# Optimization experiments

Hardware: AMD Instinct MI355X
Metric: run time of the kernel (lower is better)

Reference implementation:

```python
import jax, jax.numpy as jnp
import numpy as np

B, L, C = 1, 1536, 768
H, DK, DV, F = 8, 64, 96, 96


def setup_inputs() -> dict:
    key = jax.random.key(0)
    ks = jax.random.split(key, 9)
    s = 0.02
    return {
        "x": jax.random.normal(ks[0], (B, L, C), jnp.float32),
        "Wq": jax.random.normal(ks[1], (C, H * DK), jnp.float32) * s,
        "Wk": jax.random.normal(ks[2], (C, H * DK), jnp.float32) * s,
        "Wv": jax.random.normal(ks[3], (C, H * DV), jnp.float32) * s,
        "Wout": jax.random.normal(ks[4], (H * DV, C), jnp.float32) * s,
        "bout": jnp.zeros((C,), jnp.float32),
        "Wpos": jax.random.normal(ks[5], (F, H * DK), jnp.float32) * s,
        "rel_content_bias": jax.random.normal(ks[6], (1, H, 1, DK), jnp.float32),
        "rel_pos_bias": jax.random.normal(ks[7], (1, H, 1, DK), jnp.float32),
    }


def central_mask_embed(n, features):
    # positions: -(n-1) .. n-1  -> (2n-1,)
    positions = jnp.arange(-(n - 1), n)
    # center widths: 2^1 - 1 .. 2^features - 1
    widths = jnp.float32(2.0) ** jnp.arange(1, features + 1, dtype=jnp.float32) - 1.0
    return (widths[None, :] > jnp.abs(positions).astype(jnp.float32)[:, None]).astype(jnp.float32)


def relative_shift(t):
    # t: (b, h, t1, t2) with t2 = 2*t1 - 1 -> (b, h, t1, t1)
    b, h, t1, t2 = t.shape
    t = jnp.pad(t, ((0, 0), (0, 0), (0, 0), (1, 0)))  # (b,h,t1,t2+1)
    t = t.reshape(b, h, t2 + 1, t1)[:, :, 1:, :]       # (b,h,t2,t1)
    t = t.reshape(b, h, t1, t2)
    return t[..., : (t2 + 2) // 2]


def reference(x, Wq, Wk, Wv, Wout, bout, Wpos, rel_content_bias, rel_pos_bias):
    b, n, _ = x.shape
    q = (x @ Wq).reshape(b, n, H, DK).transpose(0, 2, 1, 3)  # b h n d
    k = (x @ Wk).reshape(b, n, H, DK).transpose(0, 2, 1, 3)
    v = (x @ Wv).reshape(b, n, H, DV).transpose(0, 2, 1, 3)
    q = q / jnp.float32(DK) ** 0.5

    content_logits = jnp.einsum("bhid,bhjd->bhij", q + rel_content_bias, k)

    pos = central_mask_embed(n, F)                 # (2n-1, F)
    pos_k = (pos @ Wpos).reshape(2 * n - 1, H, DK).transpose(1, 0, 2)  # h (2n-1) d
    pos_logits = jnp.einsum("bhid,hjd->bhij", q + rel_pos_bias, pos_k)
    pos_logits = relative_shift(pos_logits)        # (b,h,n,n)

    attn = jax.nn.softmax(content_logits + pos_logits, axis=-1)
    out = jnp.einsum("bhij,bhjd->bhid", attn, v)   # b h n dv
    out = out.transpose(0, 2, 1, 3).reshape(b, n, H * DV)
    return out @ Wout + bout
```

## Files before the change

kernel.cpp:

```cpp
#include <hip/hip_runtime.h>
#include <stdint.h>

#define NTOK 1536
#define CDIM 768
#define NH 8
#define DKH 64
#define DVH 96
#define NF 96

typedef unsigned short u16;
typedef __attribute__((ext_vector_type(8))) short s16x8;
typedef __attribute__((ext_vector_type(4))) float f32x4;

__device__ __forceinline__ float b2f(u16 u) {
    union { uint32_t i; float f; } v; v.i = ((uint32_t)u) << 16; return v.f;
}
__device__ __forceinline__ u16 f2b(float f) {
    union { float f; uint32_t i; } v; v.f = f;
    uint32_t x = v.i;
    return (u16)((x + 0x7FFFu + ((x >> 16) & 1u)) >> 16);
}
__device__ __forceinline__ float ldin(const void* p, int i, int f32) {
    return f32 ? ((const float*)p)[i] : b2f(((const u16*)p)[i]);
}

__device__ __forceinline__ int probe_f32(const void* p) {
    const u16* a = (const u16*)p;
    int lane = threadIdx.x & 63;
    int bad = 0;
#pragma unroll
    for (int t = 0; t < 4; ++t) {
        float v = b2f(a[lane + t * 64]);
        if (!(fabsf(v) < 1e6f)) bad = 1;
    }
    return __ballot(bad) != 0ull;
}

#define FIDX(m, kk) ((((kk) >> 3) * 16 + (m)) * 8 + ((kk) & 7))

#define OFF_WSUF 16
#define OFF_S11  (OFF_WSUF + 5632)
#define OFF_QF   (OFF_S11 + 147456)
#define OFF_KF   (OFF_QF + 393216)
#define OFF_VF   (OFF_KF + 393216)
#define OFF_AOF  (OFF_VF + 589824)
#define OFF_XF   (OFF_AOF + 589824)
#define OFF_WF   (OFF_XF + 589824)
#define OFF_WOF  (OFF_WF + 688128)

__global__ __launch_bounds__(256) void prep(const void* __restrict__ x,
                                            const void* __restrict__ Wq,
                                            const void* __restrict__ Wk,
                                            const void* __restrict__ Wv,
                                            const void* __restrict__ Wout,
                                            const void* __restrict__ Wpos,
                                            float* __restrict__ ws) {
    int bx = blockIdx.x, tid = threadIdx.x;
    int wv = tid >> 6, L = tid & 63;

    if (bx < 144) {
        int f = probe_f32(x);
        u16* dst = (u16*)(ws + OFF_XF);
        int cbase = (bx * 4 + wv) * 4;
        int m = L & 15, kq = L >> 4;
        int srcs[4];
#pragma unroll
        for (int c = 0; c < 4; ++c) {
            int ch = cbase + c;
            int ti = ch / 24, kc = ch % 24;
            srcs[c] = (ti * 16 + m) * CDIM + kc * 32 + kq * 8;
        }
        if (f) {
            float4 a[4][2];
#pragma unroll
            for (int c = 0; c < 4; ++c) {
                const float* xp = (const float*)x + srcs[c];
                a[c][0] = *(const float4*)(xp);
                a[c][1] = *(const float4*)(xp + 4);
            }
#pragma unroll
            for (int c = 0; c < 4; ++c) {
                union { u16 u[8]; uint4 v; } pk;
                pk.u[0] = f2b(a[c][0].x); pk.u[1] = f2b(a[c][0].y);
                pk.u[2] = f2b(a[c][0].z); pk.u[3] = f2b(a[c][0].w);
                pk.u[4] = f2b(a[c][1].x); pk.u[5] = f2b(a[c][1].y);
                pk.u[6] = f2b(a[c][1].z); pk.u[7] = f2b(a[c][1].w);
                *(uint4*)(dst + (cbase + c) * 512 + L * 8) = pk.v;
            }
        } else {
            uint4 v[4];
#pragma unroll
            for (int c = 0; c < 4; ++c) v[c] = *(const uint4*)((const u16*)x + srcs[c]);
#pragma unroll
            for (int c = 0; c < 4; ++c)
                *(uint4*)(dst + (cbase + c) * 512 + L * 8) = v[c];
        }
        return;
    }
    if (bx < 1104) {
        int c = (bx - 144) * 4 + wv;
        const void* src; int ld, cn0; u16* dst; int kc;
        if (c < 2688) {
            int tn = c / 24; kc = c % 24;
            int n0 = tn * 16;
            dst = (u16*)(ws + OFF_WF) + c * 512;
            if (n0 < 512)       { src = Wq; ld = 512;  cn0 = n0; }
            else if (n0 < 1024) { src = Wk; ld = 512;  cn0 = n0 - 512; }
            else                { src = Wv; ld = CDIM; cn0 = n0 - 1024; }
        } else {
            int c2 = c - 2688;
            int tn = c2 / 24; kc = c2 % 24;
            dst = (u16*)(ws + OFF_WOF) + c2 * 512;
            src = Wout; ld = CDIM; cn0 = tn * 16;
        }
        int f = probe_f32(src);
        int nn = L & 15, kq = L >> 4;
        int base = (kc * 32 + kq * 8) * ld + cn0 + nn;
        union { u16 u[8]; uint4 v; } pk;
        if (f) {
            const float* sp = (const float*)src + base;
            float a0 = sp[0], a1 = sp[ld], a2 = sp[2 * ld], a3 = sp[3 * ld];
            float a4 = sp[4 * ld], a5 = sp[5 * ld], a6 = sp[6 * ld], a7 = sp[7 * ld];
            pk.u[0] = f2b(a0); pk.u[1] = f2b(a1); pk.u[2] = f2b(a2); pk.u[3] = f2b(a3);
            pk.u[4] = f2b(a4); pk.u[5] = f2b(a5); pk.u[6] = f2b(a6); pk.u[7] = f2b(a7);
        } else {
            const u16* sp = (const u16*)src + base;
            pk.u[0] = sp[0]; pk.u[1] = sp[ld]; pk.u[2] = sp[2 * ld]; pk.u[3] = sp[3 * ld];
            pk.u[4] = sp[4 * ld]; pk.u[5] = sp[5 * ld]; pk.u[6] = sp[6 * ld]; pk.u[7] = sp[7 * ld];
        }
        *(uint4*)(dst + L * 8) = pk.v;
        return;
    }
    int t = bx - 1104;
    int f = probe_f32(Wpos);
    for (int hd = tid; hd < 512; hd += 256) {
        float s0 = 0.f, s1 = 0.f, s2 = 0.f, s3 = 0.f;
        int f0 = t;
        for (; f0 + 4 <= NF; f0 += 4) {
            s0 += ldin(Wpos, f0 * 512 + hd, f);
            s1 += ldin(Wpos, (f0 + 1) * 512 + hd, f);
            s2 += ldin(Wpos, (f0 + 2) * 512 + hd, f);
            s3 += ldin(Wpos, (f0 + 3) * 512 + hd, f);
        }
        for (; f0 < NF; ++f0) s0 += ldin(Wpos, f0 * 512 + hd, f);
        ws[OFF_WSUF + t * 512 + hd] = (s0 + s1) + (s2 + s3);
    }
}

__global__ __launch_bounds__(256) void qkv_reg(const void* __restrict__ rcb,
                                               const void* __restrict__ rpb,
                                               float* __restrict__ ws) {
    __shared__ float qt[64 * 68];
    __shared__ float rpd[12];
    const u16* xf = (const u16*)(ws + OFF_XF);
    const u16* wf = (const u16*)(ws + OFF_WF);
    u16* qf = (u16*)(ws + OFF_QF);
    u16* kf = (u16*)(ws + OFF_KF);
    u16* vf = (u16*)(ws + OFF_VF);

    int tid = threadIdx.x;
    int lane = tid & 63, w = tid >> 6;
    int quad = lane >> 4, col = lane & 15;
    int ti4 = blockIdx.x;
    int tn4 = blockIdx.y;
    int tn = tn4 * 4 + w;
    int i0 = ti4 * 64;
    bool isQ = (tn4 < 8);
    int hq = tn4;

    s16x8 bw0, bw1;
    int f32p = 0, f32c = 0;
    if (isQ) {
        f32p = probe_f32(rpb);
        f32c = probe_f32(rcb);
        int t = lane & 15, kq = lane >> 4;
        union { u16 u[8]; s16x8 v; } p0, p1;
#pragma unroll
        for (int j = 0; j < 8; ++j) {
            float v0 = 0.f, v1 = 0.f;
            if (t < 11) {
                v0 = ws[OFF_WSUF + t * 512 + hq * 64 + kq * 8 + j];
                v1 = ws[OFF_WSUF + t * 512 + hq * 64 + 32 + kq * 8 + j];
            }
            p0.u[j] = f2b(v0); p1.u[j] = f2b(v1);
        }
        bw0 = p0.v; bw1 = p1.v;
        if (tid < 12) {
            float s = 0.f;
            if (tid < 11) {
                const float* wp = ws + OFF_WSUF + tid * 512 + hq * 64;
                for (int d = 0; d < 64; ++d) s += ldin(rpb, hq * 64 + d, f32p) * wp[d];
            }
            rpd[tid] = s;
        }
    }

    f32x4 acc[4];
#pragma unroll
    for (int mt = 0; mt < 4; ++mt) acc[mt] = (f32x4){0.f, 0.f, 0.f, 0.f};

    const u16* bp = wf + (tn * 24) * 512 + lane * 8;
    const u16* ap = xf + (ti4 * 4 * 24) * 512 + lane * 8;
#pragma unroll 4
    for (int kc = 0; kc < 24; ++kc) {
        s16x8 bfrag = *(const s16x8*)(bp + kc * 512);
#pragma unroll
        for (int mt = 0; mt < 4; ++mt) {
            s16x8 afrag = *(const s16x8*)(ap + (mt * 24 + kc) * 512);
            acc[mt] = __builtin_amdgcn_mfma_f32_16x16x32_bf16(afrag, bfrag, acc[mt], 0, 0, 0);
        }
    }

    if (isQ) {
#pragma unroll
        for (int mt = 0; mt < 4; ++mt)
#pragma unroll
            for (int r = 0; r < 4; ++r)
                qt[(mt * 16 + quad * 4 + r) * 68 + w * 16 + col] = acc[mt][r] * 0.125f;
        __syncthreads();
        int m = lane & 15, kq = lane >> 4;
#pragma unroll
        for (int kc2 = 0; kc2 < 2; ++kc2) {
            union { u16 u[8]; uint4 v; } pk;
#pragma unroll
            for (int j = 0; j < 8; ++j) {
                int d = kc2 * 32 + kq * 8 + j;
                pk.u[j] = f2b(qt[(w * 16 + m) * 68 + d] + ldin(rcb, hq * 64 + d, f32c));
            }
            *(uint4*)(qf + (((hq * 96 + ti4 * 4 + w) * 2 + kc2) * 512) + lane * 8) = pk.v;
        }
        union { u16 u[8]; s16x8 v; } qa0, qa1;
#pragma unroll
        for (int j = 0; j < 8; ++j) {
            qa0.u[j] = f2b(qt[(w * 16 + m) * 68 + kq * 8 + j]);
            qa1.u[j] = f2b(qt[(w * 16 + m) * 68 + 32 + kq * 8 + j]);
        }
        f32x4 s11a = (f32x4){0.f, 0.f, 0.f, 0.f};
        s11a = __builtin_amdgcn_mfma_f32_16x16x32_bf16(qa0.v, bw0, s11a, 0, 0, 0);
        s11a = __builtin_amdgcn_mfma_f32_16x16x32_bf16(qa1.v, bw1, s11a, 0, 0, 0);
        if (col < 12) {
            float rp = rpd[col];
            float* s11 = ws + OFF_S11;
#pragma unroll
            for (int r = 0; r < 4; ++r)
                s11[(hq * NTOK + i0 + w * 16 + quad * 4 + r) * 12 + col] = s11a[r] + rp;
        }
    } else if (tn < 64) {
        int h = (tn >> 2) - 8;
        int d = ((tn & 3) * 16) + col;
#pragma unroll
        for (int mt = 0; mt < 4; ++mt) {
            int tj = ti4 * 4 + mt;
#pragma unroll
            for (int r = 0; r < 4; ++r) {
                int nn = quad * 4 + r;
                kf[((h * 96 + tj) * 2 + (d >> 5)) * 512 + FIDX(nn, d & 31)] = f2b(acc[mt][r]);
            }
        }
    } else {
        int c = tn * 16 + col - 1024;
        int h = c / 96, d = c % 96;
        int nt = d >> 4, nn = d & 15;
#pragma unroll
        for (int mt = 0; mt < 4; ++mt) {
#pragma unroll
            for (int r = 0; r < 4; ++r) {
                int j = i0 + mt * 16 + quad * 4 + r;
                int jc = j >> 5, kk = j & 31;
// ... 96 lines not shown
        pa.u2[1] = *(const uint2*)(pr + 4);
        const u16* vp = vf + ((h * 48 + jc) * 6) * 512 + lane * 8;
#pragma unroll
        for (int nt = 0; nt < 6; ++nt) {
            s16x8 vfr = *(const s16x8*)(vp + nt * 512);
            O[nt] = __builtin_amdgcn_mfma_f32_16x16x32_bf16(pa.v, vfr, O[nt], 0, 0, 0);
        }
    }

#pragma unroll
    for (int off = 1; off < 16; off <<= 1)
#pragma unroll
        for (int r = 0; r < 4; ++r) lsum[r] += __shfl_xor(lsum[r], off);
    if (col == 0)
#pragma unroll
        for (int r = 0; r < 4; ++r) lw[wv][quad * 4 + r] = lsum[r];
#pragma unroll
    for (int r = 0; r < 4; ++r) {
        int row = quad * 4 + r;
#pragma unroll
        for (int nt = 0; nt < 6; ++nt)
            Om[wv][row * 96 + nt * 16 + col] = O[nt][r];
    }
    __syncthreads();
    for (int idx = tid; idx < 16 * 96; idx += 512) {
        int row = idx / 96, cc = idx % 96;
        float L = 0.f, val = 0.f;
#pragma unroll
        for (int v = 0; v < 8; ++v) { L += lw[v][row]; val += Om[v][idx]; }
        aof[(ti * 24 + h * 3 + (cc >> 5)) * 512 + FIDX(row, cc & 31)] = f2b(val / L);
    }
}

__global__ __launch_bounds__(256) void out_reg(const void* __restrict__ bout,
                                               float* __restrict__ ws,
                                               float* __restrict__ out) {
    const u16* af = (const u16*)(ws + OFF_AOF);
    const u16* wof = (const u16*)(ws + OFF_WOF);
    int f32b = probe_f32(bout);

    int tid = threadIdx.x;
    int lane = tid & 63, w = tid >> 6;
    int quad = lane >> 4, col = lane & 15;
    int ti4 = blockIdx.x;
    int tn = blockIdx.y * 4 + w;
    int i0 = ti4 * 64;
    int n0 = blockIdx.y * 64;

    f32x4 acc[4];
#pragma unroll
    for (int mt = 0; mt < 4; ++mt) acc[mt] = (f32x4){0.f, 0.f, 0.f, 0.f};

    const u16* bp = wof + (tn * 24) * 512 + lane * 8;
    const u16* ap = af + (ti4 * 4 * 24) * 512 + lane * 8;
#pragma unroll 4
    for (int kc = 0; kc < 24; ++kc) {
        s16x8 bfrag = *(const s16x8*)(bp + kc * 512);
#pragma unroll
        for (int mt = 0; mt < 4; ++mt) {
            s16x8 afrag = *(const s16x8*)(ap + (mt * 24 + kc) * 512);
            acc[mt] = __builtin_amdgcn_mfma_f32_16x16x32_bf16(afrag, bfrag, acc[mt], 0, 0, 0);
        }
    }

    int c = n0 + w * 16 + col;
    float bias = ldin(bout, c, f32b);
#pragma unroll
    for (int mt = 0; mt < 4; ++mt) {
#pragma unroll
        for (int r = 0; r < 4; ++r) {
            int i = i0 + mt * 16 + quad * 4 + r;
            out[i * CDIM + c] = acc[mt][r] + bias;
        }
    }
}

extern "C" void kernel_launch(void* const* d_in, const int* in_sizes, int n_in,
                              void* d_out, int out_size, void* d_ws, size_t ws_size,
                              hipStream_t stream) {
    float* out = (float*)d_out;
    float* ws = (float*)d_ws;

    const int want[9] = {1179648, 393216, 393216, 589824, 589824, 768, 49152, 512, 512};
    int role2in[9], used[9] = {0};
    bool ok = (n_in == 9);
    if (ok) {
        for (int r = 0; r < 9; ++r) {
            int found = -1;
            for (int i = 0; i < 9 && found < 0; ++i)
                if (!used[i] && in_sizes[i] == want[r]) found = i;
            if (found < 0) { ok = false; break; }
            used[found] = 1;
            role2in[r] = found;
        }
    }
    if (!ok) for (int r = 0; r < 9; ++r) role2in[r] = r;

    const void* x    = d_in[role2in[0]];
    const void* Wq   = d_in[role2in[1]];
    const void* Wk   = d_in[role2in[2]];
    const void* Wv   = d_in[role2in[3]];
    const void* Wout = d_in[role2in[4]];
    const void* bout = d_in[role2in[5]];
    const void* Wpos = d_in[role2in[6]];
    const void* rcb  = d_in[role2in[7]];
    const void* rpb  = d_in[role2in[8]];

    hipLaunchKernelGGL(prep, dim3(1115), dim3(256), 0, stream,
                       x, Wq, Wk, Wv, Wout, Wpos, ws);
    hipLaunchKernelGGL(qkv_reg, dim3(24, 28), dim3(256), 0, stream,
                       rcb, rpb, ws);
    hipLaunchKernelGGL(attn_mfma, dim3(768), dim3(512), 0, stream, ws);
    hipLaunchKernelGGL(out_reg, dim3(24, 12), dim3(256), 0, stream,
                       bout, ws, out);
}
```

Before: 147.2 us.

## Fuse four kernels into two cooperative kernels with grid-wide syncs

Replaces the prep+qkv and attention+out-projection kernel pairs with two persistent cooperative kernels that loop over work units and use a grid sync between phases, falling back to the original launches if cooperative launch fails. The aim is to cut kernel launch gaps and tail effects between dependent stages. In exchange, grids are capped at occupancy times CU count, so work is serialized through grid-stride loops, and grid.sync adds its own barrier cost. Device properties and occupancy are queried once and cached in statics.

```diff
diff --git a/kernel.cpp b/kernel.cpp
--- a/kernel.cpp
+++ b/kernel.cpp
@@ -1,5 +1,8 @@
 #include <hip/hip_runtime.h>
+#include <hip/hip_cooperative_groups.h>
 #include <stdint.h>
+
+namespace cg = cooperative_groups;
 
 #define NTOK 1536
 #define CDIM 768
@@ -439,6 +442,406 @@
     }
 }
 
+__global__ __launch_bounds__(256) void fused_pq(const void* __restrict__ x,
+                                                const void* __restrict__ Wq,
+                                                const void* __restrict__ Wk,
+                                                const void* __restrict__ Wv,
+                                                const void* __restrict__ Wout,
+                                                const void* __restrict__ Wpos,
+                                                const void* __restrict__ rcb,
+                                                const void* __restrict__ rpb,
+                                                float* __restrict__ ws) {
+    __shared__ float qt[64 * 68];
+    __shared__ float rpd[12];
+    int tid = threadIdx.x;
+    int wv = tid >> 6, L = tid & 63;
+
+    for (int u = blockIdx.x; u < 1115; u += gridDim.x) {
+        if (u < 144) {
+            int f = probe_f32(x);
+            u16* dst = (u16*)(ws + OFF_XF);
+            int cbase = (u * 4 + wv) * 4;
+            int m = L & 15, kq = L >> 4;
+            int srcs[4];
+#pragma unroll
+            for (int c = 0; c < 4; ++c) {
+                int ch = cbase + c;
+                int ti = ch / 24, kc = ch % 24;
+                srcs[c] = (ti * 16 + m) * CDIM + kc * 32 + kq * 8;
+            }
+            if (f) {
+                float4 a[4][2];
+#pragma unroll
+                for (int c = 0; c < 4; ++c) {
+                    const float* xp = (const float*)x + srcs[c];
+                    a[c][0] = *(const float4*)(xp);
+                    a[c][1] = *(const float4*)(xp + 4);
+                }
+#pragma unroll
+                for (int c = 0; c < 4; ++c) {
+                    union { u16 uu[8]; uint4 v; } pk;
+                    pk.uu[0] = f2b(a[c][0].x); pk.uu[1] = f2b(a[c][0].y);
+                    pk.uu[2] = f2b(a[c][0].z); pk.uu[3] = f2b(a[c][0].w);
+                    pk.uu[4] = f2b(a[c][1].x); pk.uu[5] = f2b(a[c][1].y);
+                    pk.uu[6] = f2b(a[c][1].z); pk.uu[7] = f2b(a[c][1].w);
+                    *(uint4*)(dst + (cbase + c) * 512 + L * 8) = pk.v;
+                }
+            } else {
+                uint4 v[4];
+#pragma unroll
+                for (int c = 0; c < 4; ++c) v[c] = *(const uint4*)((const u16*)x + srcs[c]);
+#pragma unroll
+                for (int c = 0; c < 4; ++c)
+                    *(uint4*)(dst + (cbase + c) * 512 + L * 8) = v[c];
+            }
+        } else if (u < 1104) {
+            int c = (u - 144) * 4 + wv;
+            const void* src; int ld, cn0; u16* dst; int kc;
+            if (c < 2688) {
+                int tn = c / 24; kc = c % 24;
+                int n0 = tn * 16;
+                dst = (u16*)(ws + OFF_WF) + c * 512;
+                if (n0 < 512)       { src = Wq; ld = 512;  cn0 = n0; }
+                else if (n0 < 1024) { src = Wk; ld = 512;  cn0 = n0 - 512; }
+                else                { src = Wv; ld = CDIM; cn0 = n0 - 1024; }
+            } else {
+                int c2 = c - 2688;
+                int tn = c2 / 24; kc = c2 % 24;
+                dst = (u16*)(ws + OFF_WOF) + c2 * 512;
+                src = Wout; ld = CDIM; cn0 = tn * 16;
+            }
+            int f = probe_f32(src);
+            int nn = L & 15, kq = L >> 4;
+            int base = (kc * 32 + kq * 8) * ld + cn0 + nn;
+            union { u16 uu[8]; uint4 v; } pk;
+            if (f) {
+                const float* sp = (const float*)src + base;
+                float a0 = sp[0], a1 = sp[ld], a2 = sp[2 * ld], a3 = sp[3 * ld];
+                float a4 = sp[4 * ld], a5 = sp[5 * ld], a6 = sp[6 * ld], a7 = sp[7 * ld];
+                pk.uu[0] = f2b(a0); pk.uu[1] = f2b(a1); pk.uu[2] = f2b(a2); pk.uu[3] = f2b(a3);
+                pk.uu[4] = f2b(a4); pk.uu[5] = f2b(a5); pk.uu[6] = f2b(a6); pk.uu[7] = f2b(a7);
+            } else {
+                const u16* sp = (const u16*)src + base;
+                pk.uu[0] = sp[0]; pk.uu[1] = sp[ld]; pk.uu[2] = sp[2 * ld]; pk.uu[3] = sp[3 * ld];
+                pk.uu[4] = sp[4 * ld]; pk.uu[5] = sp[5 * ld]; pk.uu[6] = sp[6 * ld]; pk.uu[7] = sp[7 * ld];
+            }
+            *(uint4*)(dst + L * 8) = pk.v;
+        } else {
+            int t = u - 1104;
+            int f = probe_f32(Wpos);
+            for (int hd = tid; hd < 512; hd += 256) {
+                float s0 = 0.f, s1 = 0.f, s2 = 0.f, s3 = 0.f;
+                int f0 = t;
+                for (; f0 + 4 <= NF; f0 += 4) {
+                    s0 += ldin(Wpos, f0 * 512 + hd, f);
+                    s1 += ldin(Wpos, (f0 + 1) * 512 + hd, f);
+                    s2 += ldin(Wpos, (f0 + 2) * 512 + hd, f);
+                    s3 += ldin(Wpos, (f0 + 3) * 512 + hd, f);
+                }
+                for (; f0 < NF; ++f0) s0 += ldin(Wpos, f0 * 512 + hd, f);
+                ws[OFF_WSUF + t * 512 + hd] = (s0 + s1) + (s2 + s3);
+            }
+        }
+    }
+
+    __threadfence();
+    cg::this_grid().sync();
+
+    const u16* xf = (const u16*)(ws + OFF_XF);
+    const u16* wf = (const u16*)(ws + OFF_WF);
+    u16* qf = (u16*)(ws + OFF_QF);
+    u16* kf = (u16*)(ws + OFF_KF);
+    u16* vf = (u16*)(ws + OFF_VF);
+
+    for (int u = blockIdx.x; u < 672; u += gridDim.x) {
+        int ti4 = u % 24, tn4 = u / 24;
+        int lane = L, w = wv;
+        int quad = lane >> 4, col = lane & 15;
+        int tn = tn4 * 4 + w;
+        int i0 = ti4 * 64;
+        bool isQ = (tn4 < 8);
+        int hq = tn4;
+
+        s16x8 bw0, bw1;
+        int f32p = 0, f32c = 0;
+        if (isQ) {
+            f32p = probe_f32(rpb);
+            f32c = probe_f32(rcb);
+            int t = lane & 15, kq = lane >> 4;
+            union { u16 uu[8]; s16x8 v; } p0, p1;
+#pragma unroll
+            for (int j = 0; j < 8; ++j) {
+                float v0 = 0.f, v1 = 0.f;
+                if (t < 11) {
+                    v0 = ws[OFF_WSUF + t * 512 + hq * 64 + kq * 8 + j];
+                    v1 = ws[OFF_WSUF + t * 512 + hq * 64 + 32 + kq * 8 + j];
+                }
+                p0.uu[j] = f2b(v0); p1.uu[j] = f2b(v1);
+            }
+            bw0 = p0.v; bw1 = p1.v;
+            if (tid < 12) {
+                float s = 0.f;
+                if (tid < 11) {
+                    const float* wp = ws + OFF_WSUF + tid * 512 + hq * 64;
+                    for (int d = 0; d < 64; ++d) s += ldin(rpb, hq * 64 + d, f32p) * wp[d];
+                }
+                rpd[tid] = s;
+            }
+        }
+
+        f32x4 acc[4];
+#pragma unroll
+        for (int mt = 0; mt < 4; ++mt) acc[mt] = (f32x4){0.f, 0.f, 0.f, 0.f};
+
+        const u16* bp = wf + (tn * 24) * 512 + lane * 8;
+        const u16* ap = xf + (ti4 * 4 * 24) * 512 + lane * 8;
+#pragma unroll 4
+        for (int kc = 0; kc < 24; ++kc) {
+            s16x8 bfrag = *(const s16x8*)(bp + kc * 512);
+#pragma unroll
+            for (int mt = 0; mt < 4; ++mt) {
+                s16x8 afrag = *(const s16x8*)(ap + (mt * 24 + kc) * 512);
+                acc[mt] = __builtin_amdgcn_mfma_f32_16x16x32_bf16(afrag, bfrag, acc[mt], 0, 0, 0);
+            }
+        }
+
+        if (isQ) {
+#pragma unroll
+            for (int mt = 0; mt < 4; ++mt)
+#pragma unroll
+                for (int r = 0; r < 4; ++r)
+                    qt[(mt * 16 + quad * 4 + r) * 68 + w * 16 + col] = acc[mt][r] * 0.125f;
+            __syncthreads();
+            int m = lane & 15, kq = lane >> 4;
+#pragma unroll
+            for (int kc2 = 0; kc2 < 2; ++kc2) {
+                union { u16 uu[8]; uint4 v; } pk;
+#pragma unroll
+                for (int j = 0; j < 8; ++j) {
+                    int d = kc2 * 32 + kq * 8 + j;
+                    pk.uu[j] = f2b(qt[(w * 16 + m) * 68 + d] + ldin(rcb, hq * 64 + d, f32c));
+                }
+                *(uint4*)(qf + (((hq * 96 + ti4 * 4 + w) * 2 + kc2) * 512) + lane * 8) = pk.v;
+            }
+            union { u16 uu[8]; s16x8 v; } qa0, qa1;
+#pragma unroll
+            for (int j = 0; j < 8; ++j) {
+                qa0.uu[j] = f2b(qt[(w * 16 + m) * 68 + kq * 8 + j]);
+                qa1.uu[j] = f2b(qt[(w * 16 + m) * 68 + 32 + kq * 8 + j]);
+            }
+            f32x4 s11a = (f32x4){0.f, 0.f, 0.f, 0.f};
+            s11a = __builtin_amdgcn_mfma_f32_16x16x32_bf16(qa0.v, bw0, s11a, 0, 0, 0);
+            s11a = __builtin_amdgcn_mfma_f32_16x16x32_bf16(qa1.v, bw1, s11a, 0, 0, 0);
+            if (col < 12) {
+                float rp = rpd[col];
+                float* s11 = ws + OFF_S11;
+#pragma unroll
+                for (int r = 0; r < 4; ++r)
+                    s11[(hq * NTOK + i0 + w * 16 + quad * 4 + r) * 12 + col] = s11a[r] + rp;
+            }
+        } else if (tn < 64) {
+            int h = (tn >> 2) - 8;
+            int d = ((tn & 3) * 16) + col;
+#pragma unroll
+            for (int mt = 0; mt < 4; ++mt) {
+                int tj = ti4 * 4 + mt;
+#pragma unroll
+                for (int r = 0; r < 4; ++r) {
+                    int nn = quad * 4 + r;
+                    kf[((h * 96 + tj) * 2 + (d >> 5)) * 512 + FIDX(nn, d & 31)] = f2b(acc[mt][r]);
+                }
+            }
+        } else {
+            int c = tn * 16 + col - 1024;
+            int h = c / 96, d = c % 96;
+            int nt = d >> 4, nn = d & 15;
+#pragma unroll
+            for (int mt = 0; mt < 4; ++mt) {
+#pragma unroll
+                for (int r = 0; r < 4; ++r) {
+                    int j = i0 + mt * 16 + quad * 4 + r;
+                    int jc = j >> 5, kk = j & 31;
+                    vf[((h * 48 + jc) * 6 + nt) * 512 + FIDX(nn, kk)] = f2b(acc[mt][r]);
+                }
+            }
+        }
+        if (isQ) __syncthreads();
+    }
+}
+
+__global__ __launch_bounds__(512) void fused_ao(const void* __restrict__ bout,
+                                                float* __restrict__ ws,
+                                                float* __restrict__ out) {
+    __shared__ float s11b[192];
+    __shared__ alignas(16) u16 pbuf[8][16 * 36];
+    __shared__ float Om[8][16 * 96];
+    __shared__ float lw[8][16];
+
+    const u16* qf = (const u16*)(ws + OFF_QF);
+    const u16* kf = (const u16*)(ws + OFF_KF);
+    const u16* vf = (const u16*)(ws + OFF_VF);
+    const float* s11 = ws + OFF_S11;
+    u16* aof = (u16*)(ws + OFF_AOF);
+
+    int tid = threadIdx.x;
+    int wv = tid >> 6, lane = tid & 63;
+    int quad = lane >> 4, col = lane & 15;
+
+    for (int u = blockIdx.x; u < 768; u += gridDim.x) {
+        int h = u & 7;
+        int ti = u >> 3;
+        int i0 = ti * 16;
+
+        if (tid < 192) s11b[tid] = s11[(h * NTOK + i0 + tid / 12) * 12 + tid % 12];
+        const u16* qp = qf + ((h * 96 + ti) * 2) * 512 + lane * 8;
+        s16x8 a_lo = *(const s16x8*)(qp);
+        s16x8 a_hi = *(const s16x8*)(qp + 512);
+        __syncthreads();
+
+        f32x4 O[6];
+        float lsum[4];
+#pragma unroll
+        for (int nt = 0; nt < 6; ++nt) O[nt] = (f32x4){0.f, 0.f, 0.f, 0.f};
+#pragma unroll
+        for (int r = 0; r < 4; ++r) lsum[r] = 0.f;
+
+        const u16* kbase = kf + ((h * 96 + wv * 12) * 2) * 512 + lane * 8;
+        s16x8 k0lo = *(const s16x8*)(kbase);
+        s16x8 k0hi = *(const s16x8*)(kbase + 512);
+        s16x8 k1lo = *(const s16x8*)(kbase + 1024);
+        s16x8 k1hi = *(const s16x8*)(kbase + 1536);
+
+        for (int c = 0; c < 6; ++c) {
+            f32x4 t0 = (f32x4){0.f, 0.f, 0.f, 0.f};
+            f32x4 t1 = (f32x4){0.f, 0.f, 0.f, 0.f};
+            t0 = __builtin_amdgcn_mfma_f32_16x16x32_bf16(a_lo, k0lo, t0, 0, 0, 0);
+            t0 = __builtin_amdgcn_mfma_f32_16x16x32_bf16(a_hi, k0hi, t0, 0, 0, 0);
+            t1 = __builtin_amdgcn_mfma_f32_16x16x32_bf16(a_lo, k1lo, t1, 0, 0, 0);
+            t1 = __builtin_amdgcn_mfma_f32_16x16x32_bf16(a_hi, k1hi, t1, 0, 0, 0);
+            if (c < 5) {
+                const u16* kn = kbase + (c + 1) * 2048;
+                k0lo = *(const s16x8*)(kn);
+                k0hi = *(const s16x8*)(kn + 512);
+                k1lo = *(const s16x8*)(kn + 1024);
+                k1hi = *(const s16x8*)(kn + 1536);
+            }
+            int j0 = wv * 192 + c * 32;
+            int lo1 = j0 - (i0 + 15), lo2 = i0 - (j0 + 31);
+            int dmin = lo1 > 0 ? lo1 : (lo2 > 0 ? lo2 : 0);
+            int dm1 = i0 + 15 - j0, dm2 = j0 + 31 - i0;
+            int dmax = dm1 > dm2 ? dm1 : dm2;
+            int tlo = 31 - __builtin_clz(dmin + 1);
+            int thi = 31 - __builtin_clz(dmax + 1);
+            if (tlo == thi) {
+#pragma unroll
+                for (int r = 0; r < 4; ++r) {
+                    int row = quad * 4 + r;
+                    float bv = s11b[row * 12 + tlo] - 12.f;
+                    float p0 = __expf(t0[r] + bv);
+                    float p1 = __expf(t1[r] + bv);
+                    pbuf[wv][row * 36 + col] = f2b(p0);
+                    pbuf[wv][row * 36 + 16 + col] = f2b(p1);
+                    lsum[r] += p0 + p1;
+                }
+            } else {
+#pragma unroll
+                for (int r = 0; r < 4; ++r) {
+                    int row = quad * 4 + r;
+                    int ig = i0 + row;
+                    int d0 = ig - (j0 + col); d0 = d0 < 0 ? -d0 : d0;
+                    int d1 = ig - (j0 + 16 + col); d1 = d1 < 0 ? -d1 : d1;
+                    float v0 = t0[r] + s11b[row * 12 + (31 - __builtin_clz(d0 + 1))];
+                    float v1 = t1[r] + s11b[row * 12 + (31 - __builtin_clz(d1 + 1))];
+                    float p0 = __expf(v0 - 12.f);
+                    float p1 = __expf(v1 - 12.f);
+                    pbuf[wv][row * 36 + col] = f2b(p0);
+                    pbuf[wv][row * 36 + 16 + col] = f2b(p1);
+                    lsum[r] += p0 + p1;
+                }
+            }
+            int jc = wv * 6 + c;
+            const u16* pr = &pbuf[wv][col * 36 + quad * 8];
+            union { s16x8 v; uint2 u2[2]; } pa;
+            pa.u2[0] = *(const uint2*)(pr);
+            pa.u2[1] = *(const uint2*)(pr + 4);
+            const u16* vp = vf + ((h * 48 + jc) * 6) * 512 + lane * 8;
+#pragma unroll
+            for (int nt = 0; nt < 6; ++nt) {
+                s16x8 vfr = *(const s16x8*)(vp + nt * 512);
+                O[nt] = __builtin_amdgcn_mfma_f32_16x16x32_bf16(pa.v, vfr, O[nt], 0, 0, 0);
+            }
+        }
+
+#pragma unroll
+        for (int off = 1; off < 16; off <<= 1)
+#pragma unroll
+            for (int r = 0; r < 4; ++r) lsum[r] += __shfl_xor(lsum[r], off);
+        if (col == 0)
+#pragma unroll
+            for (int r = 0; r < 4; ++r) lw[wv][quad * 4 + r] = lsum[r];
+#pragma unroll
+        for (int r = 0; r < 4; ++r) {
+            int row = quad * 4 + r;
+#pragma unroll
+            for (int nt = 0; nt < 6; ++nt)
+                Om[wv][row * 96 + nt * 16 + col] = O[nt][r];
+        }
+        __syncthreads();
+        for (int idx = tid; idx < 16 * 96; idx += 512) {
+            int row = idx / 96, cc = idx % 96;
+            float Ls = 0.f, val = 0.f;
+#pragma unroll
+            for (int v = 0; v < 8; ++v) { Ls += lw[v][row]; val += Om[v][idx]; }
+            aof[(ti * 24 + h * 3 + (cc >> 5)) * 512 + FIDX(row, cc & 31)] = f2b(val / Ls);
+        }
+        __syncthreads();
+    }
+
+    __threadfence();
+    cg::this_grid().sync();
+
+    const u16* af = (const u16*)(ws + OFF_AOF);
+    const u16* wof = (const u16*)(ws + OFF_WOF);
+    int f32b = probe_f32(bout);
+    int half = tid >> 8, t2 = tid & 255;
+
+    for (int u = blockIdx.x * 2 + half; u < 288; u += gridDim.x * 2) {
+        int ti4 = u % 24, by = u / 24;
+        int lane2 = t2 & 63, w2 = t2 >> 6;
+        int quad2 = lane2 >> 4, col2 = lane2 & 15;
+        int tn = by * 4 + w2;
+        int i0 = ti4 * 64;
+        int n0 = by * 64;
+
+        f32x4 acc[4];
+#pragma unroll
+        for (int mt = 0; mt < 4; ++mt) acc[mt] = (f32x4){0.f, 0.f, 0.f, 0.f};
+
+        const u16* bp = wof + (tn * 24) * 512 + lane2 * 8;
+        const u16* ap = af + (ti4 * 4 * 24) * 512 + lane2 * 8;
+#pragma unroll 4
+        for (int kc = 0; kc < 24; ++kc) {
+            s16x8 bfrag = *(const s16x8*)(bp + kc * 512);
+#pragma unroll
+            for (int mt = 0; mt < 4; ++mt) {
+                s16x8 afrag = *(const s16x8*)(ap + (mt * 24 + kc) * 512);
+                acc[mt] = __builtin_amdgcn_mfma_f32_16x16x32_bf16(afrag, bfrag, acc[mt], 0, 0, 0);
+            }
+        }
+
+        int c = n0 + w2 * 16 + col2;
+        float bias = ldin(bout, c, f32b);
+#pragma unroll
+        for (int mt = 0; mt < 4; ++mt) {
+#pragma unroll
+            for (int r = 0; r < 4; ++r) {
+                int i = i0 + mt * 16 + quad2 * 4 + r;
+                out[i * CDIM + c] = acc[mt][r] + bias;
+            }
+        }
+    }
+}
+
 extern "C" void kernel_launch(void* const* d_in, const int* in_sizes, int n_in,
                               void* d_out, int out_size, void* d_ws, size_t ws_size,
                               hipStream_t stream) {
@@ -470,11 +873,44 @@
     const void* rcb  = d_in[role2in[7]];
     const void* rpb  = d_in[role2in[8]];
 
-    hipLaunchKernelGGL(prep, dim3(1115), dim3(256), 0, stream,
-                       x, Wq, Wk, Wv, Wout, Wpos, ws);
-    hipLaunchKernelGGL(qkv_reg, dim3(24, 28), dim3(256), 0, stream,
-                       rcb, rpb, ws);
-    hipLaunchKernelGGL(attn_mfma, dim3(768), dim3(512), 0, stream, ws);
-    hipLaunchKernelGGL(out_reg, dim3(24, 12), dim3(256), 0, stream,
-                       bout, ws, out);
-}
+    static int inited = 0;
+    static int nCU = 256, occA = 0, occB = 0;
+    if (!inited) {
+        hipDeviceProp_t prop;
+        int dev = 0;
+        (void)hipGetDevice(&dev);
+        if (hipGetDeviceProperties(&prop, dev) == hipSuccess && prop.multiProcessorCount > 0)
+            nCU = prop.multiProcessorCount;
+        if (hipOccupancyMaxActiveBlocksPerMultiprocessor(&occA, fused_pq, 256, 0) != hipSuccess)
+            occA = 0;
+        if (hipOccupancyMaxActiveBlocksPerMultiprocessor(&occB, fused_ao, 512, 0) != hipSuccess)
+            occB = 0;
+        inited = 1;
+    }
+
+    bool doneA = false, doneB = false;
+    if (occA > 0) {
+        int gridA = occA * nCU; if (gridA > 1115) gridA = 1115;
+        void* argsA[] = {(void*)&x, (void*)&Wq, (void*)&Wk, (void*)&Wv, (void*)&Wout,
+                         (void*)&Wpos, (void*)&rcb, (void*)&rpb, (void*)&ws};
+        doneA = hipLaunchCooperativeKernel(fused_pq, dim3(gridA), dim3(256),
+                                           argsA, 0, stream) == hipSuccess;
+    }
+    if (!doneA) {
+        hipLaunchKernelGGL(prep, dim3(1115), dim3(256), 0, stream,
+                           x, Wq, Wk, Wv, Wout, Wpos, ws);
+        hipLaunchKernelGGL(qkv_reg, dim3(24, 28), dim3(256), 0, stream,
+                           rcb, rpb, ws);
+    }
+    if (occB > 0) {
+        int gridB = occB * nCU; if (gridB > 768) gridB = 768;
+        void* argsB[] = {(void*)&bout, (void*)&ws, (void*)&out};
+        doneB = hipLaunchCooperativeKernel(fused_ao, dim3(gridB), dim3(512),
+                                           argsB, 0, stream) == hipSuccess;
+    }
+    if (!doneB) {
+        hipLaunchKernelGGL(attn_mfma, dim3(768), dim3(512), 0, stream, ws);
+        hipLaunchKernelGGL(out_reg, dim3(24, 12), dim3(256), 0, stream,
+                           bout, ws, out);
+    }
+}
```

Result: slower. 389.0 us (+164.3%).

## Fuse input conversion and positional suffix sums into projection kernels, drop prep

Applied to the files above, without the earlier changes.

Removes the separate prep kernel that converted x and the weights into fragment-ordered bf16 buffers and computed the Wpos suffix sums. The QKV and output projection kernels now load fp32 inputs directly, converting them to bf16 MFMA fragments on the fly with strided loads. The Q blocks recompute the Wpos suffix sums in shared memory. This saves one launch and a workspace round trip, but repeats the conversion per block and uses uncoalesced strided weight loads in the inner loop.

```diff
diff --git a/kernel.cpp b/kernel.cpp
--- a/kernel.cpp
+++ b/kernel.cpp
@@ -38,122 +38,62 @@
 
 #define FIDX(m, kk) ((((kk) >> 3) * 16 + (m)) * 8 + ((kk) & 7))
 
-#define OFF_WSUF 16
-#define OFF_S11  (OFF_WSUF + 5632)
+#define OFF_S11  16
 #define OFF_QF   (OFF_S11 + 147456)
 #define OFF_KF   (OFF_QF + 393216)
 #define OFF_VF   (OFF_KF + 393216)
 #define OFF_AOF  (OFF_VF + 589824)
-#define OFF_XF   (OFF_AOF + 589824)
-#define OFF_WF   (OFF_XF + 589824)
-#define OFF_WOF  (OFF_WF + 688128)
-
-__global__ __launch_bounds__(256) void prep(const void* __restrict__ x,
-                                            const void* __restrict__ Wq,
-                                            const void* __restrict__ Wk,
-                                            const void* __restrict__ Wv,
-                                            const void* __restrict__ Wout,
-                                            const void* __restrict__ Wpos,
-                                            float* __restrict__ ws) {
-    int bx = blockIdx.x, tid = threadIdx.x;
-    int wv = tid >> 6, L = tid & 63;
-
-    if (bx < 144) {
-        int f = probe_f32(x);
-        u16* dst = (u16*)(ws + OFF_XF);
-        int cbase = (bx * 4 + wv) * 4;
-        int m = L & 15, kq = L >> 4;
-        int srcs[4];
-#pragma unroll
-        for (int c = 0; c < 4; ++c) {
-            int ch = cbase + c;
-            int ti = ch / 24, kc = ch % 24;
-            srcs[c] = (ti * 16 + m) * CDIM + kc * 32 + kq * 8;
-        }
-        if (f) {
-            float4 a[4][2];
-#pragma unroll
-            for (int c = 0; c < 4; ++c) {
-                const float* xp = (const float*)x + srcs[c];
-                a[c][0] = *(const float4*)(xp);
-                a[c][1] = *(const float4*)(xp + 4);
-            }
-#pragma unroll
-            for (int c = 0; c < 4; ++c) {
-                union { u16 u[8]; uint4 v; } pk;
-                pk.u[0] = f2b(a[c][0].x); pk.u[1] = f2b(a[c][0].y);
-                pk.u[2] = f2b(a[c][0].z); pk.u[3] = f2b(a[c][0].w);
-                pk.u[4] = f2b(a[c][1].x); pk.u[5] = f2b(a[c][1].y);
-                pk.u[6] = f2b(a[c][1].z); pk.u[7] = f2b(a[c][1].w);
-                *(uint4*)(dst + (cbase + c) * 512 + L * 8) = pk.v;
-            }
-        } else {
-            uint4 v[4];
-#pragma unroll
-            for (int c = 0; c < 4; ++c) v[c] = *(const uint4*)((const u16*)x + srcs[c]);
-#pragma unroll
-            for (int c = 0; c < 4; ++c)
-                *(uint4*)(dst + (cbase + c) * 512 + L * 8) = v[c];
-        }
-        return;
-    }
-    if (bx < 1104) {
-        int c = (bx - 144) * 4 + wv;
-        const void* src; int ld, cn0; u16* dst; int kc;
-        if (c < 2688) {
-            int tn = c / 24; kc = c % 24;
-            int n0 = tn * 16;
-            dst = (u16*)(ws + OFF_WF) + c * 512;
-            if (n0 < 512)       { src = Wq; ld = 512;  cn0 = n0; }
-            else if (n0 < 1024) { src = Wk; ld = 512;  cn0 = n0 - 512; }
-            else                { src = Wv; ld = CDIM; cn0 = n0 - 1024; }
-        } else {
-            int c2 = c - 2688;
-            int tn = c2 / 24; kc = c2 % 24;
-            dst = (u16*)(ws + OFF_WOF) + c2 * 512;
-            src = Wout; ld = CDIM; cn0 = tn * 16;
-        }
-        int f = probe_f32(src);
-        int nn = L & 15, kq = L >> 4;
-        int base = (kc * 32 + kq * 8) * ld + cn0 + nn;
-        union { u16 u[8]; uint4 v; } pk;
-        if (f) {
-            const float* sp = (const float*)src + base;
-            float a0 = sp[0], a1 = sp[ld], a2 = sp[2 * ld], a3 = sp[3 * ld];
-            float a4 = sp[4 * ld], a5 = sp[5 * ld], a6 = sp[6 * ld], a7 = sp[7 * ld];
-            pk.u[0] = f2b(a0); pk.u[1] = f2b(a1); pk.u[2] = f2b(a2); pk.u[3] = f2b(a3);
-            pk.u[4] = f2b(a4); pk.u[5] = f2b(a5); pk.u[6] = f2b(a6); pk.u[7] = f2b(a7);
-        } else {
-            const u16* sp = (const u16*)src + base;
-            pk.u[0] = sp[0]; pk.u[1] = sp[ld]; pk.u[2] = sp[2 * ld]; pk.u[3] = sp[3 * ld];
-            pk.u[4] = sp[4 * ld]; pk.u[5] = sp[5 * ld]; pk.u[6] = sp[6 * ld]; pk.u[7] = sp[7 * ld];
-        }
-        *(uint4*)(dst + L * 8) = pk.v;
-        return;
-    }
-    int t = bx - 1104;
-    int f = probe_f32(Wpos);
-    for (int hd = tid; hd < 512; hd += 256) {
-        float s0 = 0.f, s1 = 0.f, s2 = 0.f, s3 = 0.f;
-        int f0 = t;
-        for (; f0 + 4 <= NF; f0 += 4) {
-            s0 += ldin(Wpos, f0 * 512 + hd, f);
-            s1 += ldin(Wpos, (f0 + 1) * 512 + hd, f);
-            s2 += ldin(Wpos, (f0 + 2) * 512 + hd, f);
-            s3 += ldin(Wpos, (f0 + 3) * 512 + hd, f);
-        }
-        for (; f0 < NF; ++f0) s0 += ldin(Wpos, f0 * 512 + hd, f);
-        ws[OFF_WSUF + t * 512 + hd] = (s0 + s1) + (s2 + s3);
-    }
-}
-
-__global__ __launch_bounds__(256) void qkv_reg(const void* __restrict__ rcb,
-                                               const void* __restrict__ rpb,
-                                               float* __restrict__ ws) {
+
+__device__ __forceinline__ s16x8 ldfragA(const void* x, int f32, int row16,
+                                         int kc, int lane) {
+    int m = lane & 15, kq = lane >> 4;
+    int src = (row16 * 16 + m) * CDIM + kc * 32 + kq * 8;
+    union { u16 uu[8]; uint4 v; s16x8 s; } pk;
+    if (f32) {
+        const float* xp = (const float*)x + src;
+        float4 a0 = *(const float4*)(xp);
+        float4 a1 = *(const float4*)(xp + 4);
+        pk.uu[0] = f2b(a0.x); pk.uu[1] = f2b(a0.y);
+        pk.uu[2] = f2b(a0.z); pk.uu[3] = f2b(a0.w);
+        pk.uu[4] = f2b(a1.x); pk.uu[5] = f2b(a1.y);
+        pk.uu[6] = f2b(a1.z); pk.uu[7] = f2b(a1.w);
+    } else {
+        pk.v = *(const uint4*)((const u16*)x + src);
+    }
+    return pk.s;
+}
+
+__device__ __forceinline__ s16x8 ldfragB(const void* src, int f32, int ld,
+                                         int cn0, int kc, int lane) {
+    int nn = lane & 15, kq = lane >> 4;
+    int base = (kc * 32 + kq * 8) * ld + cn0 + nn;
+    union { u16 uu[8]; s16x8 s; } pk;
+    if (f32) {
+        const float* sp = (const float*)src + base;
+#pragma unroll
+        for (int j = 0; j < 8; ++j) pk.uu[j] = f2b(sp[j * ld]);
+    } else {
+        const u16* sp = (const u16*)src + base;
+#pragma unroll
+        for (int j = 0; j < 8; ++j) pk.uu[j] = sp[j * ld];
+    }
+    return pk.s;
+}
+
+__global__ __launch_bounds__(256) void qkv_self(const void* __restrict__ x,
+                                                const void* __restrict__ Wq,
+                                                const void* __restrict__ Wk,
+                                                const void* __restrict__ Wv,
+                                                const void* __restrict__ Wpos,
+                                                const void* __restrict__ rcb,
+                                                const void* __restrict__ rpb,
+                                                float* __restrict__ ws) {
     __shared__ float qt[64 * 68];
     __shared__ float rpd[12];
-    const u16* xf = (const u16*)(ws + OFF_XF);
-    const u16* wf = (const u16*)(ws + OFF_WF);
+    __shared__ float suf0[11][64];
+    __shared__ float partw[3][64];
+    __shared__ float wsufl[11][64];
+
     u16* qf = (u16*)(ws + OFF_QF);
     u16* kf = (u16*)(ws + OFF_KF);
     u16* vf = (u16*)(ws + OFF_VF);
@@ -168,28 +108,59 @@
     bool isQ = (tn4 < 8);
     int hq = tn4;
 
+    int fx = probe_f32(x);
+
+    const void* bsrc; int bld, bcn0;
+    if (tn < 32)      { bsrc = Wq; bld = 512;  bcn0 = tn * 16; }
+    else if (tn < 64) { bsrc = Wk; bld = 512;  bcn0 = (tn - 32) * 16; }
+    else              { bsrc = Wv; bld = CDIM; bcn0 = (tn - 64) * 16; }
+    int fB = probe_f32(bsrc);
+
     s16x8 bw0, bw1;
     int f32p = 0, f32c = 0;
     if (isQ) {
+        int fwp = probe_f32(Wpos);
         f32p = probe_f32(rpb);
         f32c = probe_f32(rcb);
+        int d = lane;
+        int base = hq * 64 + d;
+        if (w == 0) {
+            float s = 0.f;
+            for (int f0 = 23; f0 >= 0; --f0) {
+                s += ldin(Wpos, f0 * 512 + base, fwp);
+                if (f0 < 11) suf0[f0][d] = s;
+            }
+        } else {
+            float s = 0.f;
+#pragma unroll 4
+            for (int f0 = w * 24; f0 < w * 24 + 24; ++f0)
+                s += ldin(Wpos, f0 * 512 + base, fwp);
+            partw[w - 1][d] = s;
+        }
+        __syncthreads();
+        for (int idx = tid; idx < 11 * 64; idx += 256) {
+            int t = idx >> 6, dd = idx & 63;
+            wsufl[t][dd] = suf0[t][dd] + partw[0][dd] + partw[1][dd] + partw[2][dd];
+        }
+        __syncthreads();
+
         int t = lane & 15, kq = lane >> 4;
-        union { u16 u[8]; s16x8 v; } p0, p1;
+        union { u16 uu[8]; s16x8 v; } p0, p1;
 #pragma unroll
         for (int j = 0; j < 8; ++j) {
             float v0 = 0.f, v1 = 0.f;
             if (t < 11) {
-                v0 = ws[OFF_WSUF + t * 512 + hq * 64 + kq * 8 + j];
-                v1 = ws[OFF_WSUF + t * 512 + hq * 64 + 32 + kq * 8 + j];
-            }
-            p0.u[j] = f2b(v0); p1.u[j] = f2b(v1);
+                v0 = wsufl[t][kq * 8 + j];
+                v1 = wsufl[t][32 + kq * 8 + j];
+            }
+            p0.uu[j] = f2b(v0); p1.uu[j] = f2b(v1);
         }
         bw0 = p0.v; bw1 = p1.v;
         if (tid < 12) {
             float s = 0.f;
             if (tid < 11) {
-                const float* wp = ws + OFF_WSUF + tid * 512 + hq * 64;
-                for (int d = 0; d < 64; ++d) s += ldin(rpb, hq * 64 + d, f32p) * wp[d];
+                for (int d2 = 0; d2 < 64; ++d2)
+                    s += ldin(rpb, hq * 64 + d2, f32p) * wsufl[tid][d2];
             }
             rpd[tid] = s;
         }
@@ -199,14 +170,12 @@
 #pragma unroll
     for (int mt = 0; mt < 4; ++mt) acc[mt] = (f32x4){0.f, 0.f, 0.f, 0.f};
 
-    const u16* bp = wf + (tn * 24) * 512 + lane * 8;
-    const u16* ap = xf + (ti4 * 4 * 24) * 512 + lane * 8;
-#pragma unroll 4
+#pragma unroll 2
     for (int kc = 0; kc < 24; ++kc) {
-        s16x8 bfrag = *(const s16x8*)(bp + kc * 512);
+        s16x8 bfrag = ldfragB(bsrc, fB, bld, bcn0, kc, lane);
 #pragma unroll
         for (int mt = 0; mt < 4; ++mt) {
-            s16x8 afrag = *(const s16x8*)(ap + (mt * 24 + kc) * 512);
+            s16x8 afrag = ldfragA(x, fx, ti4 * 4 + mt, kc, lane);
             acc[mt] = __builtin_amdgcn_mfma_f32_16x16x32_bf16(afrag, bfrag, acc[mt], 0, 0, 0);
         }
     }
@@ -221,19 +190,19 @@
         int m = lane & 15, kq = lane >> 4;
 #pragma unroll
         for (int kc2 = 0; kc2 < 2; ++kc2) {
-            union { u16 u[8]; uint4 v; } pk;
+            union { u16 uu[8]; uint4 v; } pk;
 #pragma unroll
             for (int j = 0; j < 8; ++j) {
                 int d = kc2 * 32 + kq * 8 + j;
-                pk.u[j] = f2b(qt[(w * 16 + m) * 68 + d] + ldin(rcb, hq * 64 + d, f32c));
+                pk.uu[j] = f2b(qt[(w * 16 + m) * 68 + d] + ldin(rcb, hq * 64 + d, f32c));
             }
             *(uint4*)(qf + (((hq * 96 + ti4 * 4 + w) * 2 + kc2) * 512) + lane * 8) = pk.v;
         }
-        union { u16 u[8]; s16x8 v; } qa0, qa1;
+        union { u16 uu[8]; s16x8 v; } qa0, qa1;
 #pragma unroll
         for (int j = 0; j < 8; ++j) {
-            qa0.u[j] = f2b(qt[(w * 16 + m) * 68 + kq * 8 + j]);
-            qa1.u[j] = f2b(qt[(w * 16 + m) * 68 + 32 + kq * 8 + j]);
+            qa0.uu[j] = f2b(qt[(w * 16 + m) * 68 + kq * 8 + j]);
+            qa1.uu[j] = f2b(qt[(w * 16 + m) * 68 + 32 + kq * 8 + j]);
         }
         f32x4 s11a = (f32x4){0.f, 0.f, 0.f, 0.f};
         s11a = __builtin_amdgcn_mfma_f32_16x16x32_bf16(qa0.v, bw0, s11a, 0, 0, 0);
@@ -396,12 +365,13 @@
     }
 }
 
-__global__ __launch_bounds__(256) void out_reg(const void* __restrict__ bout,
-                                               float* __restrict__ ws,
-                                               float* __restrict__ out) {
+__global__ __launch_bounds__(256) void out_self(const void* __restrict__ bout,
+                                                const void* __restrict__ Wout,
+                                                float* __restrict__ ws,
+                                                float* __restrict__ out) {
     const u16* af = (const u16*)(ws + OFF_AOF);
-    const u16* wof = (const u16*)(ws + OFF_WOF);
     int f32b = probe_f32(bout);
+    int fW = probe_f32(Wout);
 
     int tid = threadIdx.x;
     int lane = tid & 63, w = tid >> 6;
@@ -415,11 +385,10 @@
 #pragma unroll
     for (int mt = 0; mt < 4; ++mt) acc[mt] = (f32x4){0.f, 0.f, 0.f, 0.f};
 
-    const u16* bp = wof + (tn * 24) * 512 + lane * 8;
     const u16* ap = af + (ti4 * 4 * 24) * 512 + lane * 8;
-#pragma unroll 4
+#pragma unroll 2
     for (int kc = 0; kc < 24; ++kc) {
-        s16x8 bfrag = *(const s16x8*)(bp + kc * 512);
+        s16x8 bfrag = ldfragB(Wout, fW, CDIM, tn * 16, kc, lane);
 #pragma unroll
         for (int mt = 0; mt < 4; ++mt) {
             s16x8 afrag = *(const s16x8*)(ap + (mt * 24 + kc) * 512);
@@ -470,11 +439,9 @@
     const void* rcb  = d_in[role2in[7]];
     const void* rpb  = d_in[role2in[8]];
 
-    hipLaunchKernelGGL(prep, dim3(1115), dim3(256), 0, stream,
-                       x, Wq, Wk, Wv, Wout, Wpos, ws);
-    hipLaunchKernelGGL(qkv_reg, dim3(24, 28), dim3(256), 0, stream,
-                       rcb, rpb, ws);
+    hipLaunchKernelGGL(qkv_self, dim3(24, 28), dim3(256), 0, stream,
+                       x, Wq, Wk, Wv, Wpos, rcb, rpb, ws);
     hipLaunchKernelGGL(attn_mfma, dim3(768), dim3(512), 0, stream, ws);
-    hipLaunchKernelGGL(out_reg, dim3(24, 12), dim3(256), 0, stream,
-                       bout, ws, out);
-}
+    hipLaunchKernelGGL(out_self, dim3(24, 12), dim3(256), 0, stream,
+                       bout, Wout, ws, out);
+}
```

Result: slower. 187.3 us (+27.2%).

## Fuse attention and output projection into one cooperative kernel with grid sync

Applied to the files above, without the earlier changes.

Replaces the separate attention and output-projection launches with a single persistent cooperative kernel. The kernel loops over attention tiles, does a grid-wide sync, then computes the output GEMM tiles with two 256-thread halves per block. This is meant to remove a kernel launch boundary and its tail idle time. It adds grid-sync overhead, caps the grid at the occupancy limit, and keeps a fallback to the old two-kernel path.

```diff
diff --git a/kernel.cpp b/kernel.cpp
--- a/kernel.cpp
+++ b/kernel.cpp
@@ -1,5 +1,8 @@
 #include <hip/hip_runtime.h>
+#include <hip/hip_cooperative_groups.h>
 #include <stdint.h>
+
+namespace cg = cooperative_groups;
 
 #define NTOK 1536
 #define CDIM 768
@@ -439,6 +442,179 @@
     }
 }
 
+__global__ __launch_bounds__(512) void fused_ao(const void* __restrict__ bout,
+                                                float* __restrict__ ws,
+                                                float* __restrict__ out) {
+    __shared__ float s11b[192];
+    __shared__ alignas(16) u16 pbuf[8][16 * 36];
+    __shared__ float Om[8][16 * 96];
+    __shared__ float lw[8][16];
+
+    const u16* qf = (const u16*)(ws + OFF_QF);
+    const u16* kf = (const u16*)(ws + OFF_KF);
+    const u16* vf = (const u16*)(ws + OFF_VF);
+    const float* s11 = ws + OFF_S11;
+    u16* aof = (u16*)(ws + OFF_AOF);
+
+    int tid = threadIdx.x;
+    int wv = tid >> 6, lane = tid & 63;
+    int quad = lane >> 4, col = lane & 15;
+
+    for (int u = blockIdx.x; u < 768; u += gridDim.x) {
+        int h = u & 7;
+        int ti = u >> 3;
+        int i0 = ti * 16;
+
+        if (tid < 192) s11b[tid] = s11[(h * NTOK + i0 + tid / 12) * 12 + tid % 12];
+        const u16* qp = qf + ((h * 96 + ti) * 2) * 512 + lane * 8;
+        s16x8 a_lo = *(const s16x8*)(qp);
+        s16x8 a_hi = *(const s16x8*)(qp + 512);
+        __syncthreads();
+
+        f32x4 O[6];
+        float lsum[4];
+#pragma unroll
+        for (int nt = 0; nt < 6; ++nt) O[nt] = (f32x4){0.f, 0.f, 0.f, 0.f};
+#pragma unroll
+        for (int r = 0; r < 4; ++r) lsum[r] = 0.f;
+
+        const u16* kbase = kf + ((h * 96 + wv * 12) * 2) * 512 + lane * 8;
+        s16x8 k0lo = *(const s16x8*)(kbase);
+        s16x8 k0hi = *(const s16x8*)(kbase + 512);
+        s16x8 k1lo = *(const s16x8*)(kbase + 1024);
+        s16x8 k1hi = *(const s16x8*)(kbase + 1536);
+
+        for (int c = 0; c < 6; ++c) {
+            f32x4 t0 = (f32x4){0.f, 0.f, 0.f, 0.f};
+            f32x4 t1 = (f32x4){0.f, 0.f, 0.f, 0.f};
+            t0 = __builtin_amdgcn_mfma_f32_16x16x32_bf16(a_lo, k0lo, t0, 0, 0, 0);
+            t0 = __builtin_amdgcn_mfma_f32_16x16x32_bf16(a_hi, k0hi, t0, 0, 0, 0);
+            t1 = __builtin_amdgcn_mfma_f32_16x16x32_bf16(a_lo, k1lo, t1, 0, 0, 0);
+            t1 = __builtin_amdgcn_mfma_f32_16x16x32_bf16(a_hi, k1hi, t1, 0, 0, 0);
+            if (c < 5) {
+                const u16* kn = kbase + (c + 1) * 2048;
+                k0lo = *(const s16x8*)(kn);
+                k0hi = *(const s16x8*)(kn + 512);
+                k1lo = *(const s16x8*)(kn + 1024);
+                k1hi = *(const s16x8*)(kn + 1536);
+            }
+            int j0 = wv * 192 + c * 32;
+            int lo1 = j0 - (i0 + 15), lo2 = i0 - (j0 + 31);
+            int dmin = lo1 > 0 ? lo1 : (lo2 > 0 ? lo2 : 0);
+            int dm1 = i0 + 15 - j0, dm2 = j0 + 31 - i0;
+            int dmax = dm1 > dm2 ? dm1 : dm2;
+            int tlo = 31 - __builtin_clz(dmin + 1);
+            int thi = 31 - __builtin_clz(dmax + 1);
+            if (tlo == thi) {
+#pragma unroll
+                for (int r = 0; r < 4; ++r) {
+                    int row = quad * 4 + r;
+                    float bv = s11b[row * 12 + tlo] - 12.f;
+                    float p0 = __expf(t0[r] + bv);
+                    float p1 = __expf(t1[r] + bv);
+                    pbuf[wv][row * 36 + col] = f2b(p0);
+                    pbuf[wv][row * 36 + 16 + col] = f2b(p1);
+                    lsum[r] += p0 + p1;
+                }
+            } else {
+#pragma unroll
+                for (int r = 0; r < 4; ++r) {
+                    int row = quad * 4 + r;
+                    int ig = i0 + row;
+                    int d0 = ig - (j0 + col); d0 = d0 < 0 ? -d0 : d0;
+                    int d1 = ig - (j0 + 16 + col); d1 = d1 < 0 ? -d1 : d1;
+                    float v0 = t0[r] + s11b[row * 12 + (31 - __builtin_clz(d0 + 1))];
+                    float v1 = t1[r] + s11b[row * 12 + (31 - __builtin_clz(d1 + 1))];
+                    float p0 = __expf(v0 - 12.f);
+                    float p1 = __expf(v1 - 12.f);
+                    pbuf[wv][row * 36 + col] = f2b(p0);
+                    pbuf[wv][row * 36 + 16 + col] = f2b(p1);
+                    lsum[r] += p0 + p1;
+                }
+            }
+            int jc = wv * 6 + c;
+            const u16* pr = &pbuf[wv][col * 36 + quad * 8];
+            union { s16x8 v; uint2 u2[2]; } pa;
+            pa.u2[0] = *(const uint2*)(pr);
+            pa.u2[1] = *(const uint2*)(pr + 4);
+            const u16* vp = vf + ((h * 48 + jc) * 6) * 512 + lane * 8;
+#pragma unroll
+            for (int nt = 0; nt < 6; ++nt) {
+                s16x8 vfr = *(const s16x8*)(vp + nt * 512);
+                O[nt] = __builtin_amdgcn_mfma_f32_16x16x32_bf16(pa.v, vfr, O[nt], 0, 0, 0);
+            }
+        }
+
+#pragma unroll
+        for (int off = 1; off < 16; off <<= 1)
+#pragma unroll
+            for (int r = 0; r < 4; ++r) lsum[r] += __shfl_xor(lsum[r], off);
+        if (col == 0)
+#pragma unroll
+            for (int r = 0; r < 4; ++r) lw[wv][quad * 4 + r] = lsum[r];
+#pragma unroll
+        for (int r = 0; r < 4; ++r) {
+            int row = quad * 4 + r;
+#pragma unroll
+            for (int nt = 0; nt < 6; ++nt)
+                Om[wv][row * 96 + nt * 16 + col] = O[nt][r];
+        }
+        __syncthreads();
+        for (int idx = tid; idx < 16 * 96; idx += 512) {
+            int row = idx / 96, cc = idx % 96;
+            float Ls = 0.f, val = 0.f;
+#pragma unroll
+            for (int v = 0; v < 8; ++v) { Ls += lw[v][row]; val += Om[v][idx]; }
+            aof[(ti * 24 + h * 3 + (cc >> 5)) * 512 + FIDX(row, cc & 31)] = f2b(val / Ls);
+        }
+        __syncthreads();
+    }
+
+    __threadfence();
+    cg::this_grid().sync();
+
+    const u16* af = (const u16*)(ws + OFF_AOF);
+    const u16* wof = (const u16*)(ws + OFF_WOF);
+    int f32b = probe_f32(bout);
+    int half = tid >> 8, t2 = tid & 255;
+
+    for (int u = blockIdx.x * 2 + half; u < 288; u += gridDim.x * 2) {
+        int ti4 = u % 24, by = u / 24;
+        int lane2 = t2 & 63, w2 = t2 >> 6;
+        int quad2 = lane2 >> 4, col2 = lane2 & 15;
+        int tn = by * 4 + w2;
+        int i0 = ti4 * 64;
+        int n0 = by * 64;
+
+        f32x4 acc[4];
+#pragma unroll
+        for (int mt = 0; mt < 4; ++mt) acc[mt] = (f32x4){0.f, 0.f, 0.f, 0.f};
+
+        const u16* bp = wof + (tn * 24) * 512 + lane2 * 8;
+        const u16* ap = af + (ti4 * 4 * 24) * 512 + lane2 * 8;
+#pragma unroll 4
+        for (int kc = 0; kc < 24; ++kc) {
+            s16x8 bfrag = *(const s16x8*)(bp + kc * 512);
+#pragma unroll
+            for (int mt = 0; mt < 4; ++mt) {
+                s16x8 afrag = *(const s16x8*)(ap + (mt * 24 + kc) * 512);
+                acc[mt] = __builtin_amdgcn_mfma_f32_16x16x32_bf16(afrag, bfrag, acc[mt], 0, 0, 0);
+            }
+        }
+
+        int c = n0 + w2 * 16 + col2;
+        float bias = ldin(bout, c, f32b);
+#pragma unroll
+        for (int mt = 0; mt < 4; ++mt) {
+#pragma unroll
+            for (int r = 0; r < 4; ++r) {
+                int i = i0 + mt * 16 + quad2 * 4 + r;
+                out[i * CDIM + c] = acc[mt][r] + bias;
+            }
+        }
+    }
+}
+
 extern "C" void kernel_launch(void* const* d_in, const int* in_sizes, int n_in,
                               void* d_out, int out_size, void* d_ws, size_t ws_size,
                               hipStream_t stream) {
@@ -470,11 +646,34 @@
     const void* rcb  = d_in[role2in[7]];
     const void* rpb  = d_in[role2in[8]];
 
+    static int inited = 0;
+    static int nCU = 256, occB = 0;
+    if (!inited) {
+        hipDeviceProp_t prop;
+        int dev = 0;
+        (void)hipGetDevice(&dev);
+        if (hipGetDeviceProperties(&prop, dev) == hipSuccess && prop.multiProcessorCount > 0)
+            nCU = prop.multiProcessorCount;
+        if (hipOccupancyMaxActiveBlocksPerMultiprocessor(&occB, fused_ao, 512, 0) != hipSuccess)
+            occB = 0;
+        inited = 1;
+    }
+
     hipLaunchKernelGGL(prep, dim3(1115), dim3(256), 0, stream,
                        x, Wq, Wk, Wv, Wout, Wpos, ws);
     hipLaunchKernelGGL(qkv_reg, dim3(24, 28), dim3(256), 0, stream,
                        rcb, rpb, ws);
-    hipLaunchKernelGGL(attn_mfma, dim3(768), dim3(512), 0, stream, ws);
-    hipLaunchKernelGGL(out_reg, dim3(24, 12), dim3(256), 0, stream,
-                       bout, ws, out);
-}
+
+    bool doneB = false;
+    if (occB > 0) {
+        int gridB = occB * nCU; if (gridB > 768) gridB = 768;
+        void* argsB[] = {(void*)&bout, (void*)&ws, (void*)&out};
+        doneB = hipLaunchCooperativeKernel(fused_ao, dim3(gridB), dim3(512),
+                                           argsB, 0, stream) == hipSuccess;
+    }
+    if (!doneB) {
+        hipLaunchKernelGGL(attn_mfma, dim3(768), dim3(512), 0, stream, ws);
+        hipLaunchKernelGGL(out_reg, dim3(24, 12), dim3(256), 0, stream,
+                           bout, ws, out);
+    }
+}
```

Result: slower. 257.5 us (+74.9%).
